# Performance work log

Hardware: AMD Instinct MI355X
Metric: run time of the kernel (lower is better)

## Reference

```python
import jax, jax.numpy as jnp
import numpy as np

N_NODES = 50000
N_EDGES = 1600000
F_IN = 128
HIDDEN = 128
NUM_GRAPHS = 64


def _glorot(key, shape):
    fan_in = shape[0]
    return (jax.random.normal(key, shape, dtype=jnp.float32) / np.sqrt(fan_in)).astype(jnp.float32)


def setup_inputs() -> dict:
    key = jax.random.key(0)
    ks = jax.random.split(key, 16)
    x = jax.random.normal(ks[0], (N_NODES, F_IN), dtype=jnp.float32)
    edge_index = jax.random.randint(ks[1], (2, N_EDGES), 0, N_NODES, dtype=jnp.int64)
    batch = jnp.sort(jax.random.randint(ks[2], (N_NODES,), 0, NUM_GRAPHS, dtype=jnp.int64))
    # SAGEConv params: lin_l acts on aggregated neighbors, lin_r on root features.
    params = {
        'Wl0': _glorot(ks[3], (F_IN, HIDDEN)), 'Wr0': _glorot(ks[4], (F_IN, HIDDEN)), 'b0': jnp.zeros((HIDDEN,), jnp.float32),
        'Wl1': _glorot(ks[5], (HIDDEN, HIDDEN)), 'Wr1': _glorot(ks[6], (HIDDEN, HIDDEN)), 'b1': jnp.zeros((HIDDEN,), jnp.float32),
        'Wl2': _glorot(ks[7], (HIDDEN, HIDDEN)), 'Wr2': _glorot(ks[8], (HIDDEN, HIDDEN)), 'b2': jnp.zeros((HIDDEN,), jnp.float32),
        'W_lin1': _glorot(ks[9], (3 * HIDDEN, HIDDEN)), 'b_lin1': jnp.zeros((HIDDEN,), jnp.float32),
        'W_lin2': _glorot(ks[10], (HIDDEN, 2)), 'b_lin2': jnp.zeros((2,), jnp.float32),
    }
    return {'x': x, 'edge_index': edge_index, 'batch': batch, **params}


def _sage_conv(x, src, dst, Wl, Wr, b):
    # mean-aggregate neighbor (source) features at target nodes
    n = x.shape[0]
    deg = jax.ops.segment_sum(jnp.ones(src.shape, x.dtype), dst, num_segments=n)
    agg = jax.ops.segment_sum(x[src], dst, num_segments=n)
    agg = agg / jnp.maximum(deg, 1.0)[:, None]
    return agg @ Wl + x @ Wr + b


def reference(x, edge_index, batch,
              Wl0, Wr0, b0, Wl1, Wr1, b1, Wl2, Wr2, b2,
              W_lin1, b_lin1, W_lin2, b_lin2):
    src, dst = edge_index[0], edge_index[1]
    h = jax.nn.relu(_sage_conv(x, src, dst, Wl0, Wr0, b0))
    h = jax.nn.relu(_sage_conv(h, src, dst, Wl1, Wr1, b1))
    h = jax.nn.relu(_sage_conv(h, src, dst, Wl2, Wr2, b2))
    # global add / mean / max pool over graph ids
    add_p = jax.ops.segment_sum(h, batch, num_segments=NUM_GRAPHS)
    cnt = jax.ops.segment_sum(jnp.ones((h.shape[0],), h.dtype), batch, num_segments=NUM_GRAPHS)
    mean_p = add_p / jnp.maximum(cnt, 1.0)[:, None]
    max_p = jax.ops.segment_max(h, batch, num_segments=NUM_GRAPHS)
    g = jnp.concatenate([add_p, mean_p, max_p], axis=1)  # [G, 3*hidden]
    g = jax.nn.relu(g @ W_lin1 + b_lin1)
    # dropout p=0.5 is identity in eval mode
    logits = g @ W_lin2 + b_lin2
    return jax.nn.log_softmax(logits, axis=-1)
```

## Files before the change

### kernel.cpp

```cpp
#include <hip/hip_runtime.h>
#include <hip/hip_bf16.h>

#define N_NODES   50000
#define ZROW      N_NODES
#define F         128
#define NGRAPH    64
#define NB        391
#define B1        400
#define PADMAX    384

typedef __attribute__((ext_vector_type(8))) short  bf16x8;
typedef __attribute__((ext_vector_type(4))) float  f32x4;

__global__ __launch_bounds__(256) void bucket_hist(const int* __restrict__ dst,
                                                   int* __restrict__ bh, int nE, int chunk) {
    __shared__ int hist[NB];
    for (int i = threadIdx.x; i < NB; i += 256) hist[i] = 0;
    __syncthreads();
    int e0 = blockIdx.x * chunk;
    int e1 = min(e0 + chunk, nE);
    for (int e = e0 + threadIdx.x; e < e1; e += 256)
        atomicAdd(&hist[dst[e] >> 7], 1);
    __syncthreads();
    for (int i = threadIdx.x; i < NB; i += 256)
        bh[i * B1 + blockIdx.x] = hist[i];
}

__global__ __launch_bounds__(512) void scan_blocks(const int* __restrict__ bh,
                                                   int* __restrict__ boff,
                                                   int* __restrict__ btot) {
    __shared__ int s[512];
    int bkt = blockIdx.x, t = threadIdx.x;
    int v = (t < B1) ? bh[bkt * B1 + t] : 0;
    s[t] = v;
    __syncthreads();
    for (int off = 1; off < 512; off <<= 1) {
        int u = (t >= off) ? s[t - off] : 0;
        __syncthreads();
        s[t] += u;
        __syncthreads();
    }
    if (t < B1) boff[bkt * B1 + t] = s[t] - v;
    if (t == B1 - 1) btot[bkt] = s[t];
}

__global__ __launch_bounds__(512) void scan_buckets(const int* __restrict__ btot,
                                                    int* __restrict__ bbase) {
    __shared__ int s[512];
    int t = threadIdx.x;
    int v = (t < NB) ? btot[t] : 0;
    s[t] = v;
    __syncthreads();
    for (int off = 1; off < 512; off <<= 1) {
        int u = (t >= off) ? s[t - off] : 0;
        __syncthreads();
        s[t] += u;
        __syncthreads();
    }
    if (t < NB) bbase[t] = s[t] - v;
    if (t == NB - 1) bbase[NB] = s[t];
}

__global__ __launch_bounds__(256) void bucket_place(const int* __restrict__ src,
                                                    const int* __restrict__ dst,
                                                    const int* __restrict__ boff,
                                                    const int* __restrict__ bbase,
                                                    ushort2* __restrict__ ebuf, int nE, int chunk) {
    __shared__ int cur[NB];
    for (int i = threadIdx.x; i < NB; i += 256)
        cur[i] = bbase[i] + boff[i * B1 + blockIdx.x];
    __syncthreads();
    int e0 = blockIdx.x * chunk;
    int e1 = min(e0 + chunk, nE);
    for (int e = e0 + threadIdx.x; e < e1; e += 256) {
        int d = dst[e];
        int pos = atomicAdd(&cur[d >> 7], 1);
        ebuf[pos] = make_ushort2((unsigned short)src[e], (unsigned short)(d & 127));
    }
}

__global__ __launch_bounds__(256) void csr_build(const ushort2* __restrict__ ebuf,
                                                 const int* __restrict__ bbase,
                                                 int* __restrict__ row_ptr,
                                                 int* __restrict__ deg_arr,
                                                 unsigned short* __restrict__ csr, int n) {
    __shared__ int hist[128];
    __shared__ int cursor[128];
    __shared__ int pend[128];
    int b = blockIdx.x, t = threadIdx.x;
    int e0 = bbase[b], e1 = bbase[b + 1];
    if (t < 128) hist[t] = 0;
    __syncthreads();
    for (int e = e0 + t; e < e1; e += 256)
        atomicAdd(&hist[ebuf[e].y], 1);
    __syncthreads();
    if (t == 0) {
        int run = e0 + b * PADMAX;
        #pragma unroll 4
        for (int i = 0; i < 128; ++i) { cursor[i] = run; run += (hist[i] + 3) & ~3; }
    }
    __syncthreads();
    int node = b * 128 + t;
    if (t < 128) {
        pend[t] = cursor[t] + ((hist[t] + 3) & ~3);
        if (node < n) { row_ptr[node] = cursor[t]; deg_arr[node] = hist[t]; }
    }
    __syncthreads();
    for (int e = e0 + t; e < e1; e += 256) {
        ushort2 ed = ebuf[e];
        int pos = atomicAdd(&cursor[ed.y], 1);
        csr[pos] = ed.x;
    }
    __syncthreads();
    if (t < 128)
        for (int p = cursor[t]; p < pend[t]; ++p) csr[p] = (unsigned short)ZROW;
}

struct bh4 { __hip_bfloat16 a, b, c, d; };
__global__ __launch_bounds__(256) void cvt_kernel(const float* __restrict__ in,
                                                  __hip_bfloat16* __restrict__ out, long n4) {
    long i = (long)blockIdx.x * 256 + threadIdx.x;
    if (i >= n4) return;
    float4 v = ((const float4*)in)[i];
    bh4 o;
    o.a = __float2bfloat16(v.x);
    o.b = __float2bfloat16(v.y);
    o.c = __float2bfloat16(v.z);
    o.d = __float2bfloat16(v.w);
    ((bh4*)out)[i] = o;
}

__global__ __launch_bounds__(64) void zero_rows(__hip_bfloat16* __restrict__ xb,
                                                __hip_bfloat16* __restrict__ h1,
                                                __hip_bfloat16* __restrict__ h2) {
    int t = threadIdx.x;
    if (t < 48) {
        __hip_bfloat16* base = (t < 16) ? xb : (t < 32) ? h1 : h2;
        ((uint4*)(base + (long)ZROW * F))[t & 15] = make_uint4(0, 0, 0, 0);
    }
}

__global__ __launch_bounds__(256) void gather_kernel(const __hip_bfloat16* __restrict__ xin,
                                                     const int* __restrict__ row_ptr,
                                                     const int* __restrict__ deg_arr,
                                                     const unsigned short* __restrict__ csr,
                                                     __hip_bfloat16* __restrict__ agg, int n) {
    int node = blockIdx.x * 4 + (threadIdx.x >> 6);
    if (node >= n) return;
    const int lane = threadIdx.x & 63;
    const int q = lane >> 4;
    const int r = lane & 15;

    const int beg = row_ptr[node];
    const int d   = deg_arr[node];
    const int end = beg + ((d + 3) & ~3);

    const uint4* __restrict__ xr4 = (const uint4*)xin;

    float2 a0 = {0.f, 0.f}, a1 = {0.f, 0.f}, a2 = {0.f, 0.f}, a3 = {0.f, 0.f};

    #pragma unroll 2
    for (int i = beg; i < end; i += 4) {
        int s = (int)csr[i + q];
        uint4 v = xr4[(unsigned)s * 16u + r];
        a0.x += __uint_as_float(v.x << 16); a0.y += __uint_as_float(v.x & 0xffff0000u);
        a1.x += __uint_as_float(v.y << 16); a1.y += __uint_as_float(v.y & 0xffff0000u);
        a2.x += __uint_as_float(v.z << 16); a2.y += __uint_as_float(v.z & 0xffff0000u);
        a3.x += __uint_as_float(v.w << 16); a3.y += __uint_as_float(v.w & 0xffff0000u);
    }

    float v8[8] = {a0.x, a0.y, a1.x, a1.y, a2.x, a2.y, a3.x, a3.y};
    #pragma unroll
    for (int j = 0; j < 8; ++j) {
        v8[j] += __shfl_xor(v8[j], 16);
        v8[j] += __shfl_xor(v8[j], 32);
    }

    if (q == 0) {
        float inv = 1.f / fmaxf((float)d, 1.f);
        unsigned o[4];
        #pragma unroll
        for (int k = 0; k < 4; ++k) {
            __hip_bfloat16 lo = __float2bfloat16(v8[2 * k]     * inv);
            __hip_bfloat16 hi = __float2bfloat16(v8[2 * k + 1] * inv);
            o[k] = (unsigned)*(unsigned short*)&lo | ((unsigned)*(unsigned short*)&hi << 16);
        }
        ((uint4*)agg)[(long)node * 16 + r] = make_uint4(o[0], o[1], o[2], o[3]);
    }
}

__global__ __launch_bounds__(256) void wfrag_all(const float* __restrict__ Wl0, const float* __restrict__ Wr0,
                                                 const float* __restrict__ Wl1, const float* __restrict__ Wr1,
                                                 const float* __restrict__ Wl2, const float* __restrict__ Wr2,
                                                 __hip_bfloat16* __restrict__ Wf) {
    int layer = blockIdx.x >> 4;
    int t = (blockIdx.x & 15) * 256 + threadIdx.x;
    const float* Wl = (layer == 0) ? Wl0 : (layer == 1) ? Wl1 : Wl2;
    const float* Wr = (layer == 0) ? Wr0 : (layer == 1) ? Wr1 : Wr2;
    int frag = t >> 6, lane = t & 63;
    int kstep = frag >> 3, ntg = frag & 7;
    int q = lane >> 4, r = lane & 15;
    bf16x8 v;
    #pragma unroll
    for (int j = 0; j < 8; ++j) {
        int krow = kstep * 32 + q * 8 + j;
        int col  = ntg * 16 + r;
        float f  = (krow < 128) ? Wl[krow * F + col] : Wr[(krow - 128) * F + col];
        __hip_bfloat16 h = __float2bfloat16(f);
        v[j] = *(short*)&h;
    }
    ((bf16x8*)(Wf + (long)layer * 32768))[t] = v;
}

__global__ __launch_bounds__(256) void sage_gemm(const __hip_bfloat16* __restrict__ aggb,
                                                 const __hip_bfloat16* __restrict__ hinb,
                                                 const __hip_bfloat16* __restrict__ Wf,
                                                 const float* __restrict__ bias,
                                                 __hip_bfloat16* __restrict__ hout, int n) {
    __shared__ bf16x8 sW[64 * 64];

    const int tid = threadIdx.x;
    #pragma unroll
    for (int it = 0; it < 16; ++it) {
        int idx = tid + it * 256;
        sW[idx] = ((const bf16x8*)Wf)[idx];
    }
    __syncthreads();

    const int w    = tid >> 6;
    const int lane = tid & 63;
    const int wr   = w >> 1, wc = w & 1;
    const int q    = lane >> 4, r = lane & 15;
    const int m0   = blockIdx.x * 64 + wr * 32;

    int rowA0 = m0 + r;        if (rowA0 >= n) rowA0 = 0;
    int rowA1 = m0 + 16 + r;   if (rowA1 >= n) rowA1 = 0;
    const long a0 = (long)rowA0 * 128 + q * 8;
    const long a1 = (long)rowA1 * 128 + q * 8;

    f32x4 acc[2][4];
    #pragma unroll
    for (int s = 0; s < 2; ++s)
        #pragma unroll
        for (int t = 0; t < 4; ++t) acc[s][t] = (f32x4){0.f, 0.f, 0.f, 0.f};

    #pragma unroll
    for (int kstep = 0; kstep < 8; ++kstep) {
        const __hip_bfloat16* base = (kstep < 4) ? aggb : hinb;
        const int ko = (kstep & 3) * 32;
        bf16x8 af0 = *(const bf16x8*)(base + a0 + ko);
        bf16x8 af1 = *(const bf16x8*)(base + a1 + ko);
        #pragma unroll
        for (int t = 0; t < 4; ++t) {
            bf16x8 bf = sW[(kstep * 8 + wc * 4 + t) * 64 + lane];
            acc[0][t] = __builtin_amdgcn_mfma_f32_16x16x32_bf16(af0, bf, acc[0][t], 0, 0, 0);
            acc[1][t] = __builtin_amdgcn_mfma_f32_16x16x32_bf16(af1, bf, acc[1][t], 0, 0, 0);
        }
    }

    #pragma unroll
    for (int t = 0; t < 4; ++t) {
        int col = wc * 64 + t * 16 + r;
        float bv = bias[col];
        #pragma unroll
        for (int s = 0; s < 2; ++s) {
            #pragma unroll
            for (int j = 0; j < 4; ++j) {
                int rowD = m0 + s * 16 + q * 4 + j;
                if (rowD < n) {
                    float v = fmaxf(acc[s][t][j] + bv, 0.f);
                    hout[(long)rowD * F + col] = __float2bfloat16(v);
                }
            }
        }
    }
}

__global__ __launch_bounds__(128) void pool_kernel(const __hip_bfloat16* __restrict__ h,
                                                   const int* __restrict__ batch,
                                                   float* __restrict__ add_p,
                                                   unsigned* __restrict__ max_p,
                                                   float* __restrict__ cnt, int n) {
    int start = blockIdx.x * 128;
    if (start >= n) return;
    int end = min(start + 128, n);
    int c = threadIdx.x;

    float s = 0.f, mx = 0.f, ct = 0.f;
    int g = batch[start];
    for (int m = start; m < end; ++m) {
        int gm = batch[m];
        if (gm != g) {
            atomicAdd(&add_p[g * F + c], s);
            atomicMax(&max_p[g * F + c], __float_as_uint(mx));
            if (c == 0) atomicAdd(&cnt[g], ct);
            s = 0.f; mx = 0.f; ct = 0.f; g = gm;
        }
        float v = __bfloat162float(h[(long)m * F + c]);
        s += v;
        mx = fmaxf(mx, v);
        ct += 1.f;
    }
    atomicAdd(&add_p[g * F + c], s);
    atomicMax(&max_p[g * F + c], __float_as_uint(mx));
    if (c == 0) atomicAdd(&cnt[g], ct);
}

__global__ __launch_bounds__(128) void head_kernel(const float* __restrict__ add_p,
                                                   const float* __restrict__ cnt,
                                                   const unsigned* __restrict__ max_p,
                                                   const float* __restrict__ W1,
                                                   const float* __restrict__ b1,
                                                   const float* __restrict__ W2,
                                                   const float* __restrict__ b2,
                                                   float* __restrict__ out) {
    int g = blockIdx.x, n = threadIdx.x;
    __shared__ float gv[384];
    float a    = add_p[g * F + n];
    float invc = 1.f / fmaxf(cnt[g], 1.f);
    gv[n]       = a;
    gv[128 + n] = a * invc;
    gv[256 + n] = __uint_as_float(max_p[g * F + n]);
    __syncthreads();

    float acc = b1[n];
    #pragma unroll 8
    for (int k = 0; k < 384; ++k) acc += gv[k] * W1[k * F + n];
    float r = fmaxf(acc, 0.f);

    float l0 = r * W2[n * 2 + 0];
    float l1 = r * W2[n * 2 + 1];
    #pragma unroll
    for (int off = 32; off > 0; off >>= 1) {
        l0 += __shfl_down(l0, off);
        l1 += __shfl_down(l1, off);
    }
    __shared__ float part[4];
    if ((n & 63) == 0) { part[(n >> 6) * 2] = l0; part[(n >> 6) * 2 + 1] = l1; }
    __syncthreads();
    if (n == 0) {
        float L0 = part[0] + part[2] + b2[0];
        float L1 = part[1] + part[3] + b2[1];
        float m  = fmaxf(L0, L1);
        float lse = m + logf(expf(L0 - m) + expf(L1 - m));
        out[g * 2 + 0] = L0 - lse;
        out[g * 2 + 1] = L1 - lse;
    }
}

extern "C" void kernel_launch(void* const* d_in, const int* in_sizes, int n_in,
                              void* d_out, int out_size, void* d_ws, size_t ws_size,
                              hipStream_t stream) {
    const float* x     = (const float*)d_in[0];
    const int*   ei    = (const int*)d_in[1];
    const int*   batch = (const int*)d_in[2];
    const float* Wl0 = (const float*)d_in[3];
    const float* Wr0 = (const float*)d_in[4];
    const float* b0  = (const float*)d_in[5];
    const float* Wl1 = (const float*)d_in[6];
    const float* Wr1 = (const float*)d_in[7];
    const float* b1  = (const float*)d_in[8];
    const float* Wl2 = (const float*)d_in[9];
    const float* Wr2 = (const float*)d_in[10];
    const float* b2  = (const float*)d_in[11];
    const float* W_lin1 = (const float*)d_in[12];
    const float* b_lin1 = (const float*)d_in[13];
    const float* W_lin2 = (const float*)d_in[14];
    const float* b_lin2 = (const float*)d_in[15];

    const int nE = in_sizes[1] / 2;
    const int* src = ei;
    const int* dst = ei + nE;

    const long ROWS = N_NODES + 16;
    char* p = (char*)d_ws;
    int*   row_ptr = (int*)p;            p += 50048 * 4;
    int*   deg_arr = (int*)p;            p += 50048 * 4;
    unsigned short* csr = (unsigned short*)p;  p += (((long)nE + (long)NB * PADMAX + 63) & ~63L) * 2;
    int*   bh      = (int*)p;            p += ((long)NB * B1 + 16) * 4;
    int*   boff    = (int*)p;            p += ((long)NB * B1 + 16) * 4;
    int*   btot    = (int*)p;            p += 512 * 4;
    int*   bbase   = (int*)p;            p += 512 * 4;
    __hip_bfloat16* xb   = (__hip_bfloat16*)p; p += ROWS * F * 2;
    __hip_bfloat16* aggb = (__hip_bfloat16*)p; p += ROWS * F * 2;
    __hip_bfloat16* h1b  = (__hip_bfloat16*)p; p += ROWS * F * 2;
    __hip_bfloat16* h2b  = (__hip_bfloat16*)p; p += ROWS * F * 2;
    __hip_bfloat16* h3b  = (__hip_bfloat16*)p; p += ROWS * F * 2;
    __hip_bfloat16* Wf   = (__hip_bfloat16*)p; p += 3L * 32768 * 2;
    float* add_p   = (float*)p;          p += NGRAPH * F * 4;
    unsigned* max_p = (unsigned*)p;      p += NGRAPH * F * 4;
    float* cnt     = (float*)p;          p += 256;

    ushort2* ebuf = (ushort2*)aggb;

    const int chunk = (nE + B1 - 1) / B1;
    const int gridG = (N_NODES + 63) / 64;
    const int gridW = (N_NODES + 3) / 4;
    const int gridP = (N_NODES + 127) / 128;
    const int gridC = (int)(((long)N_NODES * F / 4 + 255) / 256);

    bucket_hist <<<B1, 256, 0, stream>>>(dst, bh, nE, chunk);
    scan_blocks <<<NB, 512, 0, stream>>>(bh, boff, btot);
    scan_buckets<<<1,  512, 0, stream>>>(btot, bbase);
    bucket_place<<<B1, 256, 0, stream>>>(src, dst, boff, bbase, ebuf, nE, chunk);
    csr_build   <<<NB, 256, 0, stream>>>(ebuf, bbase, row_ptr, deg_arr, csr, N_NODES);

    cvt_kernel<<<gridC, 256, 0, stream>>>(x, xb, (long)N_NODES * F / 4);
    zero_rows<<<1, 64, 0, stream>>>(xb, h1b, h2b);
    wfrag_all<<<48, 256, 0, stream>>>(Wl0, Wr0, Wl1, Wr1, Wl2, Wr2, Wf);

    gather_kernel<<<gridW, 256, 0, stream>>>(xb, row_ptr, deg_arr, csr, aggb, N_NODES);
    sage_gemm<<<gridG, 256, 0, stream>>>(aggb, xb, Wf, b0, h1b, N_NODES);
    gather_kernel<<<gridW, 256, 0, stream>>>(h1b, row_ptr, deg_arr, csr, aggb, N_NODES);
    sage_gemm<<<gridG, 256, 0, stream>>>(aggb, h1b, Wf + 32768, b1, h2b, N_NODES);
    gather_kernel<<<gridW, 256, 0, stream>>>(h2b, row_ptr, deg_arr, csr, aggb, N_NODES);
    sage_gemm<<<gridG, 256, 0, stream>>>(aggb, h2b, Wf + 65536, b2, h3b, N_NODES);

    hipMemsetAsync(add_p, 0, (NGRAPH * F * 2 + NGRAPH) * sizeof(float), stream);
    pool_kernel<<<gridP, 128, 0, stream>>>(h3b, batch, add_p, max_p, cnt, N_NODES);

    head_kernel<<<NGRAPH, 128, 0, stream>>>(add_p, cnt, max_p,
                                            W_lin1, b_lin1, W_lin2, b_lin2,
                                            (float*)d_out);
}
```

Before: 315.4 us.

## Split node features into column blocks so gathers stay cache-resident per pass

```diff
diff --git a/kernel.cpp b/kernel.cpp
--- a/kernel.cpp
+++ b/kernel.cpp
@@ -3,14 +3,17 @@
 
 #define N_NODES   50000
 #define ZROW      N_NODES
+#define ROWS      50016
+#define ROWS32    ((long)ROWS * 32)
 #define F         128
 #define NGRAPH    64
 #define NB        391
 #define B1        400
 #define PADMAX    384
 
-typedef __attribute__((ext_vector_type(8))) short  bf16x8;
-typedef __attribute__((ext_vector_type(4))) float  f32x4;
+typedef __attribute__((ext_vector_type(8))) short    bf16x8;
+typedef __attribute__((ext_vector_type(4))) float    f32x4;
+typedef __attribute__((ext_vector_type(4))) unsigned u32x4;
 
 __global__ __launch_bounds__(256) void bucket_hist(const int* __restrict__ dst,
                                                    int* __restrict__ bh, int nE, int chunk) {
@@ -118,16 +121,19 @@
 
 struct bh4 { __hip_bfloat16 a, b, c, d; };
 __global__ __launch_bounds__(256) void cvt_kernel(const float* __restrict__ in,
-                                                  __hip_bfloat16* __restrict__ out, long n4) {
-    long i = (long)blockIdx.x * 256 + threadIdx.x;
-    if (i >= n4) return;
+                                                  __hip_bfloat16* __restrict__ out) {
+    int i = blockIdx.x * 256 + threadIdx.x;
+    if (i >= N_NODES * 32) return;
+    int m  = i >> 5;
+    int c  = (i & 31) * 4;
     float4 v = ((const float4*)in)[i];
     bh4 o;
     o.a = __float2bfloat16(v.x);
     o.b = __float2bfloat16(v.y);
     o.c = __float2bfloat16(v.z);
     o.d = __float2bfloat16(v.w);
-    ((bh4*)out)[i] = o;
+    long off = (long)(c >> 5) * ROWS32 + (long)m * 32 + (c & 31);
+    *(bh4*)(out + off) = o;
 }
 
 __global__ __launch_bounds__(64) void zero_rows(__hip_bfloat16* __restrict__ xb,
@@ -136,56 +142,74 @@
     int t = threadIdx.x;
     if (t < 48) {
         __hip_bfloat16* base = (t < 16) ? xb : (t < 32) ? h1 : h2;
-        ((uint4*)(base + (long)ZROW * F))[t & 15] = make_uint4(0, 0, 0, 0);
-    }
+        int b = (t >> 2) & 3, r = t & 3;
+        ((u32x4*)(base + (long)b * ROWS32 + (long)ZROW * 32))[r] = (u32x4){0, 0, 0, 0};
+    }
+}
+
+__device__ __forceinline__ void acc8(float* a, u32x4 v) {
+    a[0] += __uint_as_float(v.x << 16); a[1] += __uint_as_float(v.x & 0xffff0000u);
+    a[2] += __uint_as_float(v.y << 16); a[3] += __uint_as_float(v.y & 0xffff0000u);
+    a[4] += __uint_as_float(v.z << 16); a[5] += __uint_as_float(v.z & 0xffff0000u);
+    a[6] += __uint_as_float(v.w << 16); a[7] += __uint_as_float(v.w & 0xffff0000u);
 }
 
 __global__ __launch_bounds__(256) void gather_kernel(const __hip_bfloat16* __restrict__ xin,
                                                      const int* __restrict__ row_ptr,
                                                      const int* __restrict__ deg_arr,
                                                      const unsigned short* __restrict__ csr,
-                                                     __hip_bfloat16* __restrict__ agg, int n) {
-    int node = blockIdx.x * 4 + (threadIdx.x >> 6);
+                                                     __hip_bfloat16* __restrict__ agg,
+                                                     int n) {
+    const int bid  = blockIdx.x;
+    const int pass = (bid & 7) >> 1;
+    const int wip  = (bid >> 3) * 2 + (bid & 1);
+    const int wave = threadIdx.x >> 6;
+    const int lane = threadIdx.x & 63;
+    const int node = wip * 16 + wave * 4 + (lane >> 4);
     if (node >= n) return;
-    const int lane = threadIdx.x & 63;
-    const int q = lane >> 4;
-    const int r = lane & 15;
-
-    const int beg = row_ptr[node];
-    const int d   = deg_arr[node];
+    const int q = (lane >> 2) & 3;
+    const int r = lane & 3;
+
+    const int beg = __builtin_nontemporal_load(&row_ptr[node]);
+    const int d   = __builtin_nontemporal_load(&deg_arr[node]);
     const int end = beg + ((d + 3) & ~3);
 
-    const uint4* __restrict__ xr4 = (const uint4*)xin;
-
-    float2 a0 = {0.f, 0.f}, a1 = {0.f, 0.f}, a2 = {0.f, 0.f}, a3 = {0.f, 0.f};
-
-    #pragma unroll 2
-    for (int i = beg; i < end; i += 4) {
-        int s = (int)csr[i + q];
-        uint4 v = xr4[(unsigned)s * 16u + r];
-        a0.x += __uint_as_float(v.x << 16); a0.y += __uint_as_float(v.x & 0xffff0000u);
-        a1.x += __uint_as_float(v.y << 16); a1.y += __uint_as_float(v.y & 0xffff0000u);
-        a2.x += __uint_as_float(v.z << 16); a2.y += __uint_as_float(v.z & 0xffff0000u);
-        a3.x += __uint_as_float(v.w << 16); a3.y += __uint_as_float(v.w & 0xffff0000u);
-    }
-
-    float v8[8] = {a0.x, a0.y, a1.x, a1.y, a2.x, a2.y, a3.x, a3.y};
+    const u32x4* __restrict__ sub = (const u32x4*)(xin + (long)pass * ROWS32);
+
+    float a[8] = {}, b[8] = {};
+    int i = beg;
+    for (; i + 7 < end; i += 8) {
+        int s0 = (int)__builtin_nontemporal_load(&csr[i + q]);
+        int s1 = (int)__builtin_nontemporal_load(&csr[i + 4 + q]);
+        u32x4 v0 = sub[(unsigned)s0 * 4u + r];
+        u32x4 v1 = sub[(unsigned)s1 * 4u + r];
+        acc8(a, v0);
+        acc8(b, v1);
+    }
+    for (; i < end; i += 4) {
+        int s0 = (int)__builtin_nontemporal_load(&csr[i + q]);
+        u32x4 v0 = sub[(unsigned)s0 * 4u + r];
+        acc8(a, v0);
+    }
+    #pragma unroll
+    for (int j = 0; j < 8; ++j) a[j] += b[j];
+
     #pragma unroll
     for (int j = 0; j < 8; ++j) {
-        v8[j] += __shfl_xor(v8[j], 16);
-        v8[j] += __shfl_xor(v8[j], 32);
-    }
-
-    if (q == 0) {
+        a[j] += __shfl_xor(a[j], 4);
+        a[j] += __shfl_xor(a[j], 8);
+    }
+
+    if ((lane & 12) == 0) {
         float inv = 1.f / fmaxf((float)d, 1.f);
-        unsigned o[4];
+        u32x4 res;
         #pragma unroll
         for (int k = 0; k < 4; ++k) {
-            __hip_bfloat16 lo = __float2bfloat16(v8[2 * k]     * inv);
-            __hip_bfloat16 hi = __float2bfloat16(v8[2 * k + 1] * inv);
-            o[k] = (unsigned)*(unsigned short*)&lo | ((unsigned)*(unsigned short*)&hi << 16);
+            __hip_bfloat16 lo = __float2bfloat16(a[2 * k]     * inv);
+            __hip_bfloat16 hi = __float2bfloat16(a[2 * k + 1] * inv);
+            res[k] = (unsigned)*(unsigned short*)&lo | ((unsigned)*(unsigned short*)&hi << 16);
         }
-        ((uint4*)agg)[(long)node * 16 + r] = make_uint4(o[0], o[1], o[2], o[3]);
+        __builtin_nontemporal_store(res, &((u32x4*)agg)[(long)node * 16 + pass * 4 + r]);
     }
 }
 
@@ -216,7 +240,8 @@
                                                  const __hip_bfloat16* __restrict__ hinb,
                                                  const __hip_bfloat16* __restrict__ Wf,
                                                  const float* __restrict__ bias,
-                                                 __hip_bfloat16* __restrict__ hout, int n) {
+                                                 __hip_bfloat16* __restrict__ hout,
+                                                 int n, int out_blocked) {
     __shared__ bf16x8 sW[64 * 64];
 
     const int tid = threadIdx.x;
@@ -235,8 +260,10 @@
 
     int rowA0 = m0 + r;        if (rowA0 >= n) rowA0 = 0;
     int rowA1 = m0 + 16 + r;   if (rowA1 >= n) rowA1 = 0;
-    const long a0 = (long)rowA0 * 128 + q * 8;
-    const long a1 = (long)rowA1 * 128 + q * 8;
+    const long agg0 = (long)rowA0 * 128 + q * 8;
+    const long agg1 = (long)rowA1 * 128 + q * 8;
+    const long hin0 = (long)rowA0 * 32 + q * 8;
+    const long hin1 = (long)rowA1 * 32 + q * 8;
 
     f32x4 acc[2][4];
     #pragma unroll
@@ -246,10 +273,16 @@
 
     #pragma unroll
     for (int kstep = 0; kstep < 8; ++kstep) {
-        const __hip_bfloat16* base = (kstep < 4) ? aggb : hinb;
-        const int ko = (kstep & 3) * 32;
-        bf16x8 af0 = *(const bf16x8*)(base + a0 + ko);
-        bf16x8 af1 = *(const bf16x8*)(base + a1 + ko);
+        bf16x8 af0, af1;
+        if (kstep < 4) {
+            const int ko = kstep * 32;
+            af0 = *(const bf16x8*)(aggb + agg0 + ko);
+            af1 = *(const bf16x8*)(aggb + agg1 + ko);
+        } else {
+            const long bo = (long)(kstep - 4) * ROWS32;
+            af0 = *(const bf16x8*)(hinb + bo + hin0);
+            af1 = *(const bf16x8*)(hinb + bo + hin1);
+        }
         #pragma unroll
         for (int t = 0; t < 4; ++t) {
             bf16x8 bf = sW[(kstep * 8 + wc * 4 + t) * 64 + lane];
@@ -262,6 +295,8 @@
     for (int t = 0; t < 4; ++t) {
         int col = wc * 64 + t * 16 + r;
         float bv = bias[col];
+        long cbase = out_blocked ? ((long)(col >> 5) * ROWS32 + (col & 31)) : (long)col;
+        long rstride = out_blocked ? 32 : 128;
         #pragma unroll
         for (int s = 0; s < 2; ++s) {
             #pragma unroll
@@ -269,7 +304,7 @@
                 int rowD = m0 + s * 16 + q * 4 + j;
                 if (rowD < n) {
                     float v = fmaxf(acc[s][t][j] + bv, 0.f);
-                    hout[(long)rowD * F + col] = __float2bfloat16(v);
+                    hout[cbase + (long)rowD * rstride] = __float2bfloat16(v);
                 }
             }
         }
@@ -372,7 +407,6 @@
     const int* src = ei;
     const int* dst = ei + nE;
 
-    const long ROWS = N_NODES + 16;
     char* p = (char*)d_ws;
     int*   row_ptr = (int*)p;            p += 50048 * 4;
     int*   deg_arr = (int*)p;            p += 50048 * 4;
@@ -381,11 +415,11 @@
     int*   boff    = (int*)p;            p += ((long)NB * B1 + 16) * 4;
     int*   btot    = (int*)p;            p += 512 * 4;
     int*   bbase   = (int*)p;            p += 512 * 4;
-    __hip_bfloat16* xb   = (__hip_bfloat16*)p; p += ROWS * F * 2;
-    __hip_bfloat16* aggb = (__hip_bfloat16*)p; p += ROWS * F * 2;
-    __hip_bfloat16* h1b  = (__hip_bfloat16*)p; p += ROWS * F * 2;
-    __hip_bfloat16* h2b  = (__hip_bfloat16*)p; p += ROWS * F * 2;
-    __hip_bfloat16* h3b  = (__hip_bfloat16*)p; p += ROWS * F * 2;
+    __hip_bfloat16* xb   = (__hip_bfloat16*)p; p += 4 * ROWS32 * 2;
+    __hip_bfloat16* aggb = (__hip_bfloat16*)p; p += 4 * ROWS32 * 2;
+    __hip_bfloat16* h1b  = (__hip_bfloat16*)p; p += 4 * ROWS32 * 2;
+    __hip_bfloat16* h2b  = (__hip_bfloat16*)p; p += 4 * ROWS32 * 2;
+    __hip_bfloat16* h3b  = (__hip_bfloat16*)p; p += 4 * ROWS32 * 2;
     __hip_bfloat16* Wf   = (__hip_bfloat16*)p; p += 3L * 32768 * 2;
     float* add_p   = (float*)p;          p += NGRAPH * F * 4;
     unsigned* max_p = (unsigned*)p;      p += NGRAPH * F * 4;
@@ -395,9 +429,9 @@
 
     const int chunk = (nE + B1 - 1) / B1;
     const int gridG = (N_NODES + 63) / 64;
-    const int gridW = (N_NODES + 3) / 4;
+    const int gridW = 12504;
     const int gridP = (N_NODES + 127) / 128;
-    const int gridC = (int)(((long)N_NODES * F / 4 + 255) / 256);
+    const int gridC = (N_NODES * 32 + 255) / 256;
 
     bucket_hist <<<B1, 256, 0, stream>>>(dst, bh, nE, chunk);
     scan_blocks <<<NB, 512, 0, stream>>>(bh, boff, btot);
@@ -405,16 +439,16 @@
     bucket_place<<<B1, 256, 0, stream>>>(src, dst, boff, bbase, ebuf, nE, chunk);
     csr_build   <<<NB, 256, 0, stream>>>(ebuf, bbase, row_ptr, deg_arr, csr, N_NODES);
 
-    cvt_kernel<<<gridC, 256, 0, stream>>>(x, xb, (long)N_NODES * F / 4);
+    cvt_kernel<<<gridC, 256, 0, stream>>>(x, xb);
     zero_rows<<<1, 64, 0, stream>>>(xb, h1b, h2b);
     wfrag_all<<<48, 256, 0, stream>>>(Wl0, Wr0, Wl1, Wr1, Wl2, Wr2, Wf);
 
     gather_kernel<<<gridW, 256, 0, stream>>>(xb, row_ptr, deg_arr, csr, aggb, N_NODES);
-    sage_gemm<<<gridG, 256, 0, stream>>>(aggb, xb, Wf, b0, h1b, N_NODES);
+    sage_gemm<<<gridG, 256, 0, stream>>>(aggb, xb, Wf, b0, h1b, N_NODES, 1);
     gather_kernel<<<gridW, 256, 0, stream>>>(h1b, row_ptr, deg_arr, csr, aggb, N_NODES);
-    sage_gemm<<<gridG, 256, 0, stream>>>(aggb, h1b, Wf + 32768, b1, h2b, N_NODES);
+    sage_gemm<<<gridG, 256, 0, stream>>>(aggb, h1b, Wf + 32768, b1, h2b, N_NODES, 1);
     gather_kernel<<<gridW, 256, 0, stream>>>(h2b, row_ptr, deg_arr, csr, aggb, N_NODES);
-    sage_gemm<<<gridG, 256, 0, stream>>>(aggb, h2b, Wf + 65536, b2, h3b, N_NODES);
+    sage_gemm<<<gridG, 256, 0, stream>>>(aggb, h2b, Wf + 65536, b2, h3b, N_NODES, 0);
 
     hipMemsetAsync(add_p, 0, (NGRAPH * F * 2 + NGRAPH) * sizeof(float), stream);
     pool_kernel<<<gridP, 128, 0, stream>>>(h3b, batch, add_p, max_p, cnt, N_NODES);
```

Measured after the change: 357.3 us. 1.13x slower.
